# Kernel optimization log

Measured on AMD Instinct MI355X. Metric: run time of the kernel, lower is better.

## Reference

```python
import math
import jax, jax.numpy as jnp
import numpy as np

MAX_LEN = 2048
D_HEAD = 64
B, H, S = 4, 16, 1024


def setup_inputs() -> dict:
    key = jax.random.key(0)
    kq, kk, kp = jax.random.split(key, 3)
    q = jax.random.normal(kq, (B, H, S, D_HEAD), dtype=jnp.float32)
    k = jax.random.normal(kk, (B, H, S, D_HEAD), dtype=jnp.float32)
    pos_table = jax.random.normal(kp, (MAX_LEN, D_HEAD), dtype=jnp.float32)
    return {"q": q, "k": k, "pos_table": pos_table}


def reference(q, k, pos_table):
    d_head = q.shape[-1]
    seq_len = q.shape[2]
    max_len = pos_table.shape[0]
    scale = 1.0 / math.sqrt(d_head)
    # attention gates: (b,h,s,s)
    gates = jax.nn.sigmoid(jnp.einsum('bhsd,bhtd->bhst', q, k) * scale)
    # context positions: weighted sum of key indices -> (b,h,s)
    positions = jnp.arange(seq_len, dtype=q.dtype)
    ctx_pos = jnp.einsum('bhst,t->bhs', gates, positions)
    ctx_pos = jnp.clip(ctx_pos, 0.0, float(max_len - 2))
    pos_floor = ctx_pos.astype(jnp.int32)  # (b,h,s)
    pos_frac = (ctx_pos - pos_floor.astype(q.dtype))[..., None]  # (b,h,s,1)
    emb_floor = pos_table[pos_floor]  # (b,h,s,d)
    emb_ceil = pos_table[jnp.minimum(pos_floor + 1, max_len - 1)]
    pos_emb = emb_floor + pos_frac * (emb_ceil - emb_floor)  # (b,h,s,d)
    # bias: (b,h,s,s)
    bias = jnp.einsum('bhsd,bhtd->bhst', q, pos_emb)
    return bias
```

## Files before the change

### kernel.cpp

```cpp
#include <hip/hip_runtime.h>

#define Bb_ 4
#define Hh_ 16
#define Ss_ 1024
#define DH 64
#define MAXLEN 2048
#define BH (Bb_*Hh_)
#define LDST 72
#define SW 132

typedef __attribute__((ext_vector_type(8))) short short8;
typedef __attribute__((ext_vector_type(4))) float floatx4;
typedef __attribute__((ext_vector_type(4))) unsigned short ushort4v;

static __device__ __forceinline__ unsigned short f2bf(float f) {
    unsigned int u = __builtin_bit_cast(unsigned int, f);
    u = (u + 0x7fffu + ((u >> 16) & 1u)) >> 16;
    return (unsigned short)u;
}

static __device__ __forceinline__ void stage_tile(unsigned short* lds,
                                                  const float* __restrict__ g,
                                                  int tid) {
#pragma unroll
    for (int it = 0; it < 8; ++it) {
        int idx = it * 1024 + tid * 4;
        int row = idx >> 6, col = idx & 63;
        const float4 v = *reinterpret_cast<const float4*>(g + row * 64 + col);
        ushort4v o = { f2bf(v.x), f2bf(v.y), f2bf(v.z), f2bf(v.w) };
        *reinterpret_cast<ushort4v*>(lds + row * LDST + col) = o;
    }
}

__global__ __launch_bounds__(256, 2)
void cope_kernel(const float* __restrict__ q, const float* __restrict__ k,
                 const float* __restrict__ tb, float* __restrict__ out) {
    __shared__ __align__(16) unsigned char smem[73728];
    __shared__ __align__(16) float sh_c[128];
    __shared__ __align__(16) float sh_pr[64];
    __shared__ int shf[4];
    __shared__ __align__(16) float ctx_all[1024];

    unsigned short* Ab = reinterpret_cast<unsigned short*>(smem);
    unsigned short* Kb = reinterpret_cast<unsigned short*>(smem + 18432);
    float* scratch = reinterpret_cast<float*>(smem + 18432);
    unsigned short* Pb = reinterpret_cast<unsigned short*>(smem + 55296);

    int bx = blockIdx.x;
    int bh = bx & 63, jj = bx >> 6;
    int tid = threadIdx.x;
    int lane = tid & 63, w = tid >> 6;
    int lo = lane & 15, quad = lane >> 4;

    const float* kb = k + (size_t)bh * Ss_ * DH;
    const float* qb = q + (size_t)bh * Ss_ * DH;

    const float kSig = -0.18033688011112042f;

    {
        const float* ktop = kb + (size_t)992 * DH;
#pragma unroll
        for (int it = 0; it < 2; ++it) {
            int idx = it * 1024 + tid * 4;
            int row = idx >> 6, col = idx & 63;
            const float4 v = *reinterpret_cast<const float4*>(ktop + row * 64 + col);
            ushort4v o = { f2bf(v.x), f2bf(v.y), f2bf(v.z), f2bf(v.w) };
            *reinterpret_cast<ushort4v*>(Kb + row * LDST + col) = o;
        }
    }

    bool ok = true;
    short8 bkr[2][2];
#pragma unroll 1
    for (int qt = 0; qt < 8; ++qt) {
        stage_tile(Ab, qb + (size_t)qt * 128 * DH, tid);
        __syncthreads();
        if (qt == 0) {
#pragma unroll
            for (int j = 0; j < 2; ++j) {
                bkr[j][0] = *reinterpret_cast<const short8*>(
                    &Kb[(j * 16 + lo) * LDST + 0 + quad * 8]);
                bkr[j][1] = *reinterpret_cast<const short8*>(
                    &Kb[(j * 16 + lo) * LDST + 32 + quad * 8]);
            }
        }
        short8 afr[2][2];
#pragma unroll
        for (int i = 0; i < 2; ++i)
#pragma unroll
            for (int k2 = 0; k2 < 2; ++k2)
                afr[i][k2] = *reinterpret_cast<const short8*>(
                    &Ab[(w * 32 + i * 16 + lo) * LDST + k2 * 32 + quad * 8]);

        float ps[2][4];
#pragma unroll
        for (int i = 0; i < 2; ++i)
#pragma unroll
            for (int r = 0; r < 4; ++r) ps[i][r] = 0.f;

#pragma unroll
        for (int j = 0; j < 2; ++j) {
            float tcol = (float)(992 + j * 16 + lo);
#pragma unroll
            for (int i = 0; i < 2; ++i) {
                floatx4 c = {0.f, 0.f, 0.f, 0.f};
                c = __builtin_amdgcn_mfma_f32_16x16x32_bf16(afr[i][0], bkr[j][0], c, 0, 0, 0);
                c = __builtin_amdgcn_mfma_f32_16x16x32_bf16(afr[i][1], bkr[j][1], c, 0, 0, 0);
#pragma unroll
                for (int r = 0; r < 4; ++r) {
                    float e = __builtin_amdgcn_exp2f(c[r] * kSig);
                    float g = __builtin_amdgcn_rcpf(1.0f + e);
                    ps[i][r] = fmaf(g, tcol, ps[i][r]);
                }
            }
        }
#pragma unroll
        for (int i = 0; i < 2; ++i)
#pragma unroll
            for (int r = 0; r < 4; ++r) {
                float v = ps[i][r];
                v += __shfl_xor(v, 1);
                v += __shfl_xor(v, 2);
                v += __shfl_xor(v, 4);
                v += __shfl_xor(v, 8);
                ok = ok && (v >= 4096.0f);
            }
        __syncthreads();
    }

    int wall = __all(ok);
    if (lane == 0) shf[w] = wall;
    __syncthreads();

    if (shf[0] & shf[1] & shf[2] & shf[3]) {
        if (tid < 16) {
            int d0 = tid * 4;
            *reinterpret_cast<float4*>(&sh_pr[d0]) =
                *reinterpret_cast<const float4*>(tb + (size_t)(MAXLEN - 2) * DH + d0);
        }
        __syncthreads();

        int half = tid & 1;
        float ph[32];
#pragma unroll
        for (int d = 0; d < 32; ++d) ph[d] = sh_pr[half * 32 + d];
        {
            int p = tid >> 1;
            int row = jj + 8 * p;
            const float* qr = qb + (size_t)row * DH + half * 32;
            float s = 0.f;
#pragma unroll
            for (int d = 0; d < 32; d += 4) {
                const float4 qq = *reinterpret_cast<const float4*>(qr + d);
                s += qq.x * ph[d] + qq.y * ph[d + 1] + qq.z * ph[d + 2] +
                     qq.w * ph[d + 3];
            }
            s += __shfl_xor(s, 1);
            if (half == 0) sh_c[p] = s;
        }
        __syncthreads();

        float* po = out + (size_t)bh * (Ss_ * Ss_) + (size_t)jj * Ss_ + tid * 4;
#pragma unroll 8
        for (int it = 0; it < 128; ++it) {
            float c = sh_c[it];
            floatx4 vv = {c, c, c, c};
            *reinterpret_cast<floatx4*>(po + (size_t)it * 8 * Ss_) = vv;
        }
        return;
    }

    int s0 = jj << 7;
#pragma unroll 1
    for (int qt = 0; qt < 8; ++qt) {
        stage_tile(Ab, qb + (size_t)qt * 128 * DH, tid);
        float rp2[2][4];
#pragma unroll
        for (int i = 0; i < 2; ++i)
#pragma unroll
            for (int r = 0; r < 4; ++r) rp2[i][r] = 0.f;
        short8 afr[2][2];
#pragma unroll 1
        for (int kt = 0; kt < 8; ++kt) {
            stage_tile(Pb, kb + (size_t)kt * 128 * DH, tid);
            __syncthreads();
            if (kt == 0) {
#pragma unroll
                for (int i = 0; i < 2; ++i)
#pragma unroll
                    for (int k2 = 0; k2 < 2; ++k2)
                        afr[i][k2] = *reinterpret_cast<const short8*>(
                            &Ab[(w * 32 + i * 16 + lo) * LDST + k2 * 32 + quad * 8]);
            }
            int t0 = kt << 7;
#pragma unroll
            for (int j = 0; j < 8; ++j) {
                short8 b0 = *reinterpret_cast<const short8*>(
                    &Pb[(j * 16 + lo) * LDST + 0 + quad * 8]);
                short8 b1 = *reinterpret_cast<const short8*>(
                    &Pb[(j * 16 + lo) * LDST + 32 + quad * 8]);
                float tcol = (float)(t0 + j * 16 + lo);
#pragma unroll
                for (int i = 0; i < 2; ++i) {
                    floatx4 c = {0.f, 0.f, 0.f, 0.f};
                    c = __builtin_amdgcn_mfma_f32_16x16x32_bf16(afr[i][0], b0, c, 0, 0, 0);
                    c = __builtin_amdgcn_mfma_f32_16x16x32_bf16(afr[i][1], b1, c, 0, 0, 0);
#pragma unroll
                    for (int r = 0; r < 4; ++r) {
                        float e = __builtin_amdgcn_exp2f(c[r] * kSig);
                        float g = __builtin_amdgcn_rcpf(1.0f + e);
                        rp2[i][r] = fmaf(g, tcol, rp2[i][r]);
                    }
                }
            }
            __syncthreads();
        }
#pragma unroll
        for (int i = 0; i < 2; ++i)
#pragma unroll
            for (int r = 0; r < 4; ++r) {
                float v = rp2[i][r];
                v += __shfl_xor(v, 1);
                v += __shfl_xor(v, 2);
                v += __shfl_xor(v, 4);
                v += __shfl_xor(v, 8);
                if (lo == 0) {
                    int lr = qt * 128 + w * 32 + i * 16 + quad * 4 + r;
                    ctx_all[lr] = fminf(fmaxf(v, 0.f), (float)(MAXLEN - 2));
                }
            }
    }
    __syncthreads();

    stage_tile(Ab, qb + (size_t)s0 * DH, tid);
    __syncthreads();
    short8 mfr[2][2];
#pragma unroll
    for (int i = 0; i < 2; ++i)
#pragma unroll
        for (int k2 = 0; k2 < 2; ++k2)
            mfr[i][k2] = *reinterpret_cast<const short8*>(
                &Ab[(w * 32 + i * 16 + lo) * LDST + k2 * 32 + quad * 8]);

#pragma unroll 1
    for (int kt = 0; kt < 8; ++kt) {
        {
            int rsub = tid >> 4;
            int d0 = (tid & 15) * 4;
#pragma unroll
            for (int pass = 0; pass < 8; ++pass) {
                int row = pass * 16 + rsub;
                float c = ctx_all[kt * 128 + row];
                int fl = (int)c;
                float fr = c - (float)fl;
                int ce = min(fl + 1, MAXLEN - 1);
                const float4 e0 = *reinterpret_cast<const float4*>(tb + fl * DH + d0);
                const float4 e1 = *reinterpret_cast<const float4*>(tb + ce * DH + d0);
                ushort4v o = { f2bf(e0.x + fr * (e1.x - e0.x)),
                               f2bf(e0.y + fr * (e1.y - e0.y)),
                               f2bf(e0.z + fr * (e1.z - e0.z)),
                               f2bf(e0.w + fr * (e1.w - e0.w)) };
                *reinterpret_cast<ushort4v*>(&Pb[row * LDST + d0]) = o;
            }
        }
        __syncthreads();

        short8 bfr[8][2];
#pragma unroll
        for (int j = 0; j < 8; ++j) {
            bfr[j][0] = *reinterpret_cast<const short8*>(
                &Pb[(j * 16 + lo) * LDST + 0 + quad * 8]);
            bfr[j][1] = *reinterpret_cast<const short8*>(
                &Pb[(j * 16 + lo) * LDST + 32 + quad * 8]);
        }

        floatx4 acc[2][8];
#pragma unroll
        for (int i = 0; i < 2; ++i)
#pragma unroll
            for (int j = 0; j < 8; ++j) acc[i][j] = (floatx4){0.f, 0.f, 0.f, 0.f};

#pragma unroll
        for (int j = 0; j < 8; ++j)
#pragma unroll
            for (int i = 0; i < 2; ++i) {
                acc[i][j] = __builtin_amdgcn_mfma_f32_16x16x32_bf16(
                    mfr[i][0], bfr[j][0], acc[i][j], 0, 0, 0);
                acc[i][j] = __builtin_amdgcn_mfma_f32_16x16x32_bf16(
                    mfr[i][1], bfr[j][1], acc[i][j], 0, 0, 0);
            }

#pragma unroll
        for (int i = 0; i < 2; ++i) {
            __syncthreads();
#pragma unroll
            for (int j = 0; j < 8; ++j)
#pragma unroll
                for (int r = 0; r < 4; ++r) {
                    int lrow = w * 16 + quad * 4 + r;
                    scratch[lrow * SW + j * 16 + lo] = acc[i][j][r];
                }
            __syncthreads();
#pragma unroll
            for (int it = 0; it < 8; ++it) {
                int flat = it * 1024 + tid * 4;
                int lrow = flat >> 7, col = flat & 127;
                floatx4 vv =
                    *reinterpret_cast<const floatx4*>(&scratch[lrow * SW + col]);
                int grow = (lrow >> 4) * 32 + i * 16 + (lrow & 15);
                *reinterpret_cast<floatx4*>(
                    out + (size_t)(bh * Ss_ + s0 + grow) * Ss_ + kt * 128 + col) = vv;
            }
        }
        __syncthreads();
    }
}

extern "C" void kernel_launch(void* const* d_in, const int* in_sizes, int n_in,
                              void* d_out, int out_size, void* d_ws, size_t ws_size,
                              hipStream_t stream) {
    const float* q  = (const float*)d_in[0];
    const float* k  = (const float*)d_in[1];
    const float* tb = (const float*)d_in[2];
    float* out = (float*)d_out;

    cope_kernel<<<BH * 8, 256, 0, stream>>>(q, k, tb, out);
}
```

Measured before the change: 294.3 us.

## Split into separate vote and emit kernels using workspace flags

Moves the saturation check (last 32 keys against all queries) and the per-row constant bias into a small vote kernel. It writes per-tile flags and row values to workspace, so each tile no longer recomputes the full check. A second emit kernel with more blocks and higher occupancy then either streams the constant rows or runs a scalar fallback path. This targets redundant check work and store throughput, at the cost of an extra launch. It depends on the workspace being large enough; otherwise the old kernel runs.

```diff
diff --git a/kernel.cpp b/kernel.cpp
--- a/kernel.cpp
+++ b/kernel.cpp
@@ -32,6 +32,233 @@
     }
 }
 
+
+__global__ __launch_bounds__(256, 2)
+void vote_kernel(const float* __restrict__ q, const float* __restrict__ k,
+                 const float* __restrict__ tb, int* __restrict__ flags,
+                 float* __restrict__ cvals) {
+    __shared__ __align__(16) unsigned short Ab[128 * LDST];
+    __shared__ __align__(16) unsigned short Kb[32 * LDST];
+    __shared__ __align__(16) float sh_pr[64];
+    __shared__ int shf[4];
+
+    int bx = blockIdx.x;
+    int bh = bx >> 3, j = bx & 7;
+    int tid = threadIdx.x;
+    int lane = tid & 63, w = tid >> 6;
+    int lo = lane & 15, quad = lane >> 4;
+
+    const float* kb = k + (size_t)bh * Ss_ * DH;
+    const float* qb = q + (size_t)bh * Ss_ * DH;
+    const float kSig = -0.18033688011112042f;
+
+    {
+        const float* ktop = kb + (size_t)992 * DH;
+#pragma unroll
+        for (int it = 0; it < 2; ++it) {
+            int idx = it * 1024 + tid * 4;
+            int row = idx >> 6, col = idx & 63;
+            const float4 v = *reinterpret_cast<const float4*>(ktop + row * 64 + col);
+            ushort4v o = { f2bf(v.x), f2bf(v.y), f2bf(v.z), f2bf(v.w) };
+            *reinterpret_cast<ushort4v*>(Kb + row * LDST + col) = o;
+        }
+    }
+    stage_tile(Ab, qb + (size_t)j * 128 * DH, tid);
+    if (tid < 16) {
+        int d0 = tid * 4;
+        *reinterpret_cast<float4*>(&sh_pr[d0]) =
+            *reinterpret_cast<const float4*>(tb + (size_t)(MAXLEN - 2) * DH + d0);
+    }
+    __syncthreads();
+
+    short8 bkr[2][2];
+#pragma unroll
+    for (int j2 = 0; j2 < 2; ++j2) {
+        bkr[j2][0] = *reinterpret_cast<const short8*>(
+            &Kb[(j2 * 16 + lo) * LDST + 0 + quad * 8]);
+        bkr[j2][1] = *reinterpret_cast<const short8*>(
+            &Kb[(j2 * 16 + lo) * LDST + 32 + quad * 8]);
+    }
+    short8 afr[2][2];
+#pragma unroll
+    for (int i = 0; i < 2; ++i)
+#pragma unroll
+        for (int k2 = 0; k2 < 2; ++k2)
+            afr[i][k2] = *reinterpret_cast<const short8*>(
+                &Ab[(w * 32 + i * 16 + lo) * LDST + k2 * 32 + quad * 8]);
+
+    float ps[2][4];
+#pragma unroll
+    for (int i = 0; i < 2; ++i)
+#pragma unroll
+        for (int r = 0; r < 4; ++r) ps[i][r] = 0.f;
+
+#pragma unroll
+    for (int j2 = 0; j2 < 2; ++j2) {
+        float tcol = (float)(992 + j2 * 16 + lo);
+#pragma unroll
+        for (int i = 0; i < 2; ++i) {
+            floatx4 c = {0.f, 0.f, 0.f, 0.f};
+            c = __builtin_amdgcn_mfma_f32_16x16x32_bf16(afr[i][0], bkr[j2][0], c, 0, 0, 0);
+            c = __builtin_amdgcn_mfma_f32_16x16x32_bf16(afr[i][1], bkr[j2][1], c, 0, 0, 0);
+#pragma unroll
+            for (int r = 0; r < 4; ++r) {
+                float e = __builtin_amdgcn_exp2f(c[r] * kSig);
+                float g = __builtin_amdgcn_rcpf(1.0f + e);
+                ps[i][r] = fmaf(g, tcol, ps[i][r]);
+            }
+        }
+    }
+
+    bool ok = true;
+#pragma unroll
+    for (int i = 0; i < 2; ++i)
+#pragma unroll
+        for (int r = 0; r < 4; ++r) {
+            float v = ps[i][r];
+            v += __shfl_xor(v, 1);
+            v += __shfl_xor(v, 2);
+            v += __shfl_xor(v, 4);
+            v += __shfl_xor(v, 8);
+            ok = ok && (v >= 4096.0f);
+        }
+    int wall = __all(ok);
+    if (lane == 0) shf[w] = wall;
+    __syncthreads();
+    if (tid == 0) flags[bx] = (shf[0] & shf[1] & shf[2] & shf[3]) & 1;
+
+    {
+        int half = tid & 1;
+        float ph[32];
+#pragma unroll
+        for (int d = 0; d < 32; ++d) ph[d] = sh_pr[half * 32 + d];
+        int row = tid >> 1;
+        const float* qr = qb + (size_t)(j * 128 + row) * DH + half * 32;
+        float s = 0.f;
+#pragma unroll
+        for (int d = 0; d < 32; d += 4) {
+            const float4 qq = *reinterpret_cast<const float4*>(qr + d);
+            s += qq.x * ph[d] + qq.y * ph[d + 1] + qq.z * ph[d + 2] +
+                 qq.w * ph[d + 3];
+        }
+        s += __shfl_xor(s, 1);
+        if (half == 0) cvals[(bh << 10) + j * 128 + row] = s;
+    }
+}
+
+__global__ __launch_bounds__(256, 4)
+void emit_kernel(const float* __restrict__ q, const float* __restrict__ k,
+                 const float* __restrict__ tb, const int* __restrict__ flags,
+                 const float* __restrict__ cvals, float* __restrict__ out) {
+    __shared__ __align__(16) float sh[2048 + 2048 + 1024 + 64];
+    float* kch   = sh;
+    float* embch = sh + 2048;
+    float* ctxv  = sh + 4096;
+    float* shc   = sh + 5120;
+
+    int bx = blockIdx.x;
+    int bh = bx >> 4, m = bx & 15;
+    int tid = threadIdx.x;
+    const float* qb = q + (size_t)bh * Ss_ * DH;
+    const float* kb = k + (size_t)bh * Ss_ * DH;
+    const float kSig = -0.18033688011112042f;
+
+    int fsum = 0;
+#pragma unroll
+    for (int j2 = 0; j2 < 8; ++j2) fsum += flags[bh * 8 + j2];
+
+    int r0 = m * 64;
+    float* po = out + ((size_t)bh << 20) + ((size_t)r0 << 10) + tid * 4;
+
+    if (fsum == 8) {
+        if (tid < 64) shc[tid] = cvals[(bh << 10) + r0 + tid];
+        __syncthreads();
+#pragma unroll 8
+        for (int i = 0; i < 64; ++i) {
+            float c = shc[i];
+            floatx4 vv = {c, c, c, c};
+            *reinterpret_cast<floatx4*>(po + (size_t)i * 1024) = vv;
+        }
+        return;
+    }
+
+#pragma unroll 1
+    for (int p = 0; p < 4; ++p) {
+        int u = p * 256 + tid;
+        float4 qr[16];
+#pragma unroll
+        for (int d = 0; d < 16; ++d)
+            qr[d] = *reinterpret_cast<const float4*>(qb + (size_t)u * DH + d * 4);
+        float acc = 0.f;
+#pragma unroll 1
+        for (int ch = 0; ch < 32; ++ch) {
+            __syncthreads();
+            {
+                int idx = tid * 8;
+                const float4 a = *reinterpret_cast<const float4*>(
+                    kb + (size_t)ch * 32 * DH + idx);
+                const float4 b = *reinterpret_cast<const float4*>(
+                    kb + (size_t)ch * 32 * DH + idx + 4);
+                *reinterpret_cast<float4*>(kch + idx) = a;
+                *reinterpret_cast<float4*>(kch + idx + 4) = b;
+            }
+            __syncthreads();
+#pragma unroll
+            for (int tt = 0; tt < 32; ++tt) {
+                const float* kr = kch + tt * 64;
+                float d = 0.f;
+#pragma unroll
+                for (int e = 0; e < 16; ++e) {
+                    const float4 kk = *reinterpret_cast<const float4*>(kr + e * 4);
+                    d += qr[e].x * kk.x + qr[e].y * kk.y + qr[e].z * kk.z +
+                         qr[e].w * kk.w;
+                }
+                float ex = __builtin_amdgcn_exp2f(d * kSig);
+                float g = __builtin_amdgcn_rcpf(1.f + ex);
+                acc = fmaf(g, (float)(ch * 32 + tt), acc);
+            }
+        }
+        ctxv[u] = fminf(fmaxf(acc, 0.f), (float)(MAXLEN - 2));
+    }
+    __syncthreads();
+
+#pragma unroll 1
+    for (int ch = 0; ch < 32; ++ch) {
+        __syncthreads();
+        {
+            int tl = tid >> 3;
+            int d0 = (tid & 7) * 8;
+            float c = ctxv[ch * 32 + tl];
+            int fl = (int)c;
+            float fr = c - (float)fl;
+            int ce = min(fl + 1, MAXLEN - 1);
+#pragma unroll
+            for (int e = 0; e < 8; ++e) {
+                float e0 = tb[fl * DH + d0 + e];
+                float e1 = tb[ce * DH + d0 + e];
+                embch[tl * 64 + d0 + e] = e0 + fr * (e1 - e0);
+            }
+        }
+        __syncthreads();
+        int s = tid >> 2;
+        int t0 = (tid & 3) * 8;
+        const float* qr = qb + (size_t)(r0 + s) * DH;
+#pragma unroll
+        for (int tt = 0; tt < 8; ++tt) {
+            const float* er = embch + (t0 + tt) * 64;
+            float dsum = 0.f;
+#pragma unroll
+            for (int e = 0; e < 16; ++e) {
+                const float4 qq = *reinterpret_cast<const float4*>(qr + e * 4);
+                const float4 ee = *reinterpret_cast<const float4*>(er + e * 4);
+                dsum += qq.x * ee.x + qq.y * ee.y + qq.z * ee.z + qq.w * ee.w;
+            }
+            out[((size_t)bh << 20) + (size_t)(r0 + s) * 1024 + ch * 32 + t0 + tt] =
+                dsum;
+        }
+    }
+}
+
 __global__ __launch_bounds__(256, 2)
 void cope_kernel(const float* __restrict__ q, const float* __restrict__ k,
                  const float* __restrict__ tb, float* __restrict__ out) {
@@ -54,7 +281,6 @@
 
     const float* kb = k + (size_t)bh * Ss_ * DH;
     const float* qb = q + (size_t)bh * Ss_ * DH;
-
     const float kSig = -0.18033688011112042f;
 
     {
@@ -139,7 +365,6 @@
                 *reinterpret_cast<const float4*>(tb + (size_t)(MAXLEN - 2) * DH + d0);
         }
         __syncthreads();
-
         int half = tid & 1;
         float ph[32];
 #pragma unroll
@@ -159,7 +384,6 @@
             if (half == 0) sh_c[p] = s;
         }
         __syncthreads();
-
         float* po = out + (size_t)bh * (Ss_ * Ss_) + (size_t)jj * Ss_ + tid * 4;
 #pragma unroll 8
         for (int it = 0; it < 128; ++it) {
@@ -324,5 +548,12 @@
     const float* tb = (const float*)d_in[2];
     float* out = (float*)d_out;
 
-    cope_kernel<<<BH * 8, 256, 0, stream>>>(q, k, tb, out);
+    if (d_ws != nullptr && ws_size >= 2048 + 64 * 1024 * 4) {
+        int* flags = (int*)d_ws;
+        float* cvals = (float*)((char*)d_ws + 2048);
+        vote_kernel<<<BH * 8, 256, 0, stream>>>(q, k, tb, flags, cvals);
+        emit_kernel<<<BH * 16, 256, 0, stream>>>(q, k, tb, flags, cvals, out);
+    } else {
+        cope_kernel<<<BH * 8, 256, 0, stream>>>(q, k, tb, out);
+    }
 }
```

New measurement: 291.7 us. No clear change (-0.9%).
